# Optimization experiments

Measured on AMD Instinct MI355X. Metric: run time of the kernel, lower is better.

The kernel has to match this reference:

```python
import jax, jax.numpy as jnp
import numpy as np

IN_DIM = 5000
OUT_DIM = 30
K = 50
BATCH = 16384


def setup_inputs() -> dict:
    key = jax.random.key(0)
    ks = jax.random.split(key, 8)
    return {
        "x": jax.random.normal(ks[0], (BATCH, IN_DIM), dtype=jnp.float32),
        "logits": jax.random.normal(ks[1], (IN_DIM,), dtype=jnp.float32),
        "W1": jax.random.normal(ks[2], (IN_DIM, 32), dtype=jnp.float32) * (1.0 / np.sqrt(IN_DIM)),
        "b1": jax.random.normal(ks[3], (32,), dtype=jnp.float32) * 0.01,
        "W2": jax.random.normal(ks[4], (32, 16), dtype=jnp.float32) * (1.0 / np.sqrt(32)),
        "b2": jax.random.normal(ks[5], (16,), dtype=jnp.float32) * 0.01,
        "W3": jax.random.normal(ks[6], (16, OUT_DIM), dtype=jnp.float32) * (1.0 / np.sqrt(16)),
        "b3": jax.random.normal(ks[7], (OUT_DIM,), dtype=jnp.float32) * 0.01,
        "epoch": 10,
        "total_epochs": 100,
    }


def reference(x, logits, W1, b1, W2, b2, W3, b3, epoch, total_epochs):
    # Eval path (training=False): top-k one-hot mask over the learned logits.
    # indices of top-k logits -> k-hot mask of shape [in_dim]
    _, idx = jax.lax.top_k(logits, K)                 # [K]
    mask = jnp.zeros_like(logits).at[idx].set(1.0)    # [in_dim], k-hot
    xm = mask * x                                      # [B, in_dim] gated input
    h = jax.nn.relu(xm @ W1 + b1)                      # [B, 32]
    h = jax.nn.relu(h @ W2 + b2)                       # [B, 16]
    out = h @ W3 + b3                                  # [B, out_dim]
    return out, mask
```

## Files before the change

### kernel.cpp

```cpp
#include <hip/hip_runtime.h>
#include <hip/hip_bf16.h>

#define N_IN 5000
#define K_SEL 50
#define B_ROWS 16384
#define OUT_D 30

__global__ __launch_bounds__(256) void topk_mask_kernel(
    const float* __restrict__ logits,
    float* __restrict__ mask,
    int* __restrict__ idx_out)
{
    __shared__ unsigned int s_cnt[36];
    __shared__ int s_tick, s_sel;

    const int tid  = threadIdx.x;
    const int lane = tid & 63;

    if (tid < 36) s_cnt[tid] = 0u;
    if (tid == 40) s_tick = 0;
    if (tid == 41) s_sel = 0;

    unsigned int key[20];
#pragma unroll
    for (int j = 0; j < 20; j++) {
        int i = tid + j * 256;
        if (i < N_IN) {
            unsigned int b = __float_as_uint(logits[i]);
            key[j] = (b & 0x80000000u) ? ~b : (b | 0x80000000u);
            mask[i] = 0.0f;
        } else {
            key[j] = 0u;
        }
    }
    __syncthreads();

    unsigned int lo = 0u, hi = 0xFFFFFFFFu;
    bool exact = false;
    unsigned int T;
    for (int iter = 0; iter < 32; iter++) {
        if (lo >= hi) break;
        unsigned int mid = lo + ((hi - lo) >> 1) + 1u;
        unsigned int c = 0;
#pragma unroll
        for (int j = 0; j < 20; j++) c += (key[j] >= mid) ? 1u : 0u;
#pragma unroll
        for (int off = 32; off > 0; off >>= 1) c += __shfl_down(c, off, 64);
        if (lane == 0) atomicAdd(&s_cnt[iter], c);
        __syncthreads();
        unsigned int cnt = s_cnt[iter];
        if (cnt == (unsigned)K_SEL) { T = mid; exact = true; break; }
        if (cnt > (unsigned)K_SEL) lo = mid; else hi = mid - 1u;
    }

    if (exact) {
#pragma unroll
        for (int j = 0; j < 20; j++) {
            int i = tid + j * 256;
            if (i < N_IN && key[j] >= T) {
                int slot = atomicAdd(&s_sel, 1);
                idx_out[slot] = i;
                mask[i] = 1.0f;
            }
        }
        return;
    }

    const unsigned int KT = lo;
    {
        unsigned int c = 0;
#pragma unroll
        for (int j = 0; j < 20; j++) c += (key[j] > KT) ? 1u : 0u;
#pragma unroll
        for (int off = 32; off > 0; off >>= 1) c += __shfl_down(c, off, 64);
        if (lane == 0) atomicAdd(&s_cnt[35], c);
    }
    __syncthreads();
    const int rem = K_SEL - (int)s_cnt[35];

#pragma unroll
    for (int j = 0; j < 20; j++) {
        int i = tid + j * 256;
        if (i >= N_IN) continue;
        unsigned int k = key[j];
        bool sel = false;
        if (k > KT) sel = true;
        else if (k == KT) { int t = atomicAdd(&s_tick, 1); sel = (t < rem); }
        if (sel) {
            int slot = atomicAdd(&s_sel, 1);
            idx_out[slot] = i;
            mask[i] = 1.0f;
        }
    }
}

__global__ __launch_bounds__(256) void gated_mlp_kernel(
    const float* __restrict__ x,
    const float* __restrict__ W1,
    const float* __restrict__ b1,
    const float* __restrict__ W2,
    const float* __restrict__ b2,
    const float* __restrict__ W3,
    const float* __restrict__ b3,
    const int* __restrict__ idx,
    float* __restrict__ out)
{
    __shared__ float xs[64 * 51];
    __shared__ float h1s[64 * 33];
    __shared__ float h2s[64 * 17];
    __shared__ float sW1[K_SEL * 32];
    __shared__ float sW2[32 * 16];
    __shared__ float sW3[16 * OUT_D];
    __shared__ float sb1[32];
    __shared__ float sb2[16];
    __shared__ float sb3[OUT_D];
    __shared__ int   sidx[K_SEL];

    const int tid = threadIdx.x;

    if (tid < K_SEL) sidx[tid] = idx[tid];
    for (int e = tid; e < K_SEL * 32; e += 256) {
        int k = e >> 5, j = e & 31;
        sW1[e] = W1[(size_t)idx[k] * 32 + j];
    }
    for (int e = tid; e < 32 * 16; e += 256) sW2[e] = W2[e];
    for (int e = tid; e < 16 * OUT_D; e += 256) sW3[e] = W3[e];
    if (tid < 32) sb1[tid] = b1[tid];
    if (tid < 16) sb2[tid] = b2[tid];
    if (tid < OUT_D) sb3[tid] = b3[tid];
    __syncthreads();

    {
        const int r = tid >> 2;
        const int q = tid & 3;
        const int row = blockIdx.x * 64 + r;
        const float* __restrict__ xrow = x + (size_t)row * N_IN;
        float g[13];
#pragma unroll
        for (int u = 0; u < 13; u++) {
            int k = q * 13 + u;
            if (k < K_SEL) g[u] = xrow[sidx[k]];
        }
#pragma unroll
        for (int u = 0; u < 13; u++) {
            int k = q * 13 + u;
            if (k < K_SEL) xs[r * 51 + k] = g[u];
        }
    }
    __syncthreads();

    const int r = tid & 63;
    const int c = tid >> 6;

    {
        float acc[8];
#pragma unroll
        for (int jj = 0; jj < 8; jj++) acc[jj] = sb1[c * 8 + jj];
        const float* xr = &xs[r * 51];
        for (int k = 0; k < K_SEL; k++) {
            float xk = xr[k];
            const float* w = &sW1[k * 32 + c * 8];
#pragma unroll
            for (int jj = 0; jj < 8; jj++) acc[jj] = fmaf(xk, w[jj], acc[jj]);
        }
#pragma unroll
        for (int jj = 0; jj < 8; jj++) h1s[r * 33 + c * 8 + jj] = fmaxf(acc[jj], 0.0f);
    }
    __syncthreads();

    {
        float acc[4];
#pragma unroll
        for (int jj = 0; jj < 4; jj++) acc[jj] = sb2[c * 4 + jj];
        const float* hr = &h1s[r * 33];
#pragma unroll
        for (int i = 0; i < 32; i++) {
            float a = hr[i];
            const float* w = &sW2[i * 16 + c * 4];
#pragma unroll
            for (int jj = 0; jj < 4; jj++) acc[jj] = fmaf(a, w[jj], acc[jj]);
        }
#pragma unroll
        for (int jj = 0; jj < 4; jj++) h2s[r * 17 + c * 4 + jj] = fmaxf(acc[jj], 0.0f);
    }
    __syncthreads();

    {
        const int j0 = c * 8;
        const int nj = (c == 3) ? 6 : 8;
        float acc[8];
        for (int jj = 0; jj < nj; jj++) acc[jj] = sb3[j0 + jj];
        const float* hr = &h2s[r * 17];
#pragma unroll
        for (int i = 0; i < 16; i++) {
            float a = hr[i];
            const float* w = &sW3[i * OUT_D + j0];
            for (int jj = 0; jj < nj; jj++) acc[jj] = fmaf(a, w[jj], acc[jj]);
        }
        float* so = xs;
        for (int jj = 0; jj < nj; jj++) so[r * OUT_D + j0 + jj] = acc[jj];
    }
    __syncthreads();

    {
        float4* out4 = (float4*)(out + (size_t)blockIdx.x * 64 * OUT_D);
        const float4* so4 = (const float4*)xs;
        for (int e = tid; e < (64 * OUT_D) / 4; e += 256) out4[e] = so4[e];
    }
}

extern "C" void kernel_launch(void* const* d_in, const int* in_sizes, int n_in,
                              void* d_out, int out_size, void* d_ws, size_t ws_size,
                              hipStream_t stream) {
    const float* x      = (const float*)d_in[0];
    const float* logits = (const float*)d_in[1];
    const float* W1     = (const float*)d_in[2];
    const float* b1     = (const float*)d_in[3];
    const float* W2     = (const float*)d_in[4];
    const float* b2     = (const float*)d_in[5];
    const float* W3     = (const float*)d_in[6];
    const float* b3     = (const float*)d_in[7];

    float* out  = (float*)d_out;
    float* mask = out + (size_t)B_ROWS * OUT_D;
    int*   idx  = (int*)d_ws;

    topk_mask_kernel<<<1, 256, 0, stream>>>(logits, mask, idx);
    gated_mlp_kernel<<<256, 256, 0, stream>>>(x, W1, b1, W2, b2, W3, b3, idx, out);
}
```

Measured before the change: 424.1 us.

## Fuse top-k selection into the MLP kernel, recomputing it per block

Measured after the change: 421.3 us. No clear change (-0.7%).

```diff
diff --git a/kernel.cpp b/kernel.cpp
--- a/kernel.cpp
+++ b/kernel.cpp
@@ -6,104 +6,17 @@
 #define B_ROWS 16384
 #define OUT_D 30
 
-__global__ __launch_bounds__(256) void topk_mask_kernel(
+__global__ __launch_bounds__(256) void fused_gated_mlp_kernel(
+    const float* __restrict__ x,
     const float* __restrict__ logits,
-    float* __restrict__ mask,
-    int* __restrict__ idx_out)
-{
-    __shared__ unsigned int s_cnt[36];
-    __shared__ int s_tick, s_sel;
-
-    const int tid  = threadIdx.x;
-    const int lane = tid & 63;
-
-    if (tid < 36) s_cnt[tid] = 0u;
-    if (tid == 40) s_tick = 0;
-    if (tid == 41) s_sel = 0;
-
-    unsigned int key[20];
-#pragma unroll
-    for (int j = 0; j < 20; j++) {
-        int i = tid + j * 256;
-        if (i < N_IN) {
-            unsigned int b = __float_as_uint(logits[i]);
-            key[j] = (b & 0x80000000u) ? ~b : (b | 0x80000000u);
-            mask[i] = 0.0f;
-        } else {
-            key[j] = 0u;
-        }
-    }
-    __syncthreads();
-
-    unsigned int lo = 0u, hi = 0xFFFFFFFFu;
-    bool exact = false;
-    unsigned int T;
-    for (int iter = 0; iter < 32; iter++) {
-        if (lo >= hi) break;
-        unsigned int mid = lo + ((hi - lo) >> 1) + 1u;
-        unsigned int c = 0;
-#pragma unroll
-        for (int j = 0; j < 20; j++) c += (key[j] >= mid) ? 1u : 0u;
-#pragma unroll
-        for (int off = 32; off > 0; off >>= 1) c += __shfl_down(c, off, 64);
-        if (lane == 0) atomicAdd(&s_cnt[iter], c);
-        __syncthreads();
-        unsigned int cnt = s_cnt[iter];
-        if (cnt == (unsigned)K_SEL) { T = mid; exact = true; break; }
-        if (cnt > (unsigned)K_SEL) lo = mid; else hi = mid - 1u;
-    }
-
-    if (exact) {
-#pragma unroll
-        for (int j = 0; j < 20; j++) {
-            int i = tid + j * 256;
-            if (i < N_IN && key[j] >= T) {
-                int slot = atomicAdd(&s_sel, 1);
-                idx_out[slot] = i;
-                mask[i] = 1.0f;
-            }
-        }
-        return;
-    }
-
-    const unsigned int KT = lo;
-    {
-        unsigned int c = 0;
-#pragma unroll
-        for (int j = 0; j < 20; j++) c += (key[j] > KT) ? 1u : 0u;
-#pragma unroll
-        for (int off = 32; off > 0; off >>= 1) c += __shfl_down(c, off, 64);
-        if (lane == 0) atomicAdd(&s_cnt[35], c);
-    }
-    __syncthreads();
-    const int rem = K_SEL - (int)s_cnt[35];
-
-#pragma unroll
-    for (int j = 0; j < 20; j++) {
-        int i = tid + j * 256;
-        if (i >= N_IN) continue;
-        unsigned int k = key[j];
-        bool sel = false;
-        if (k > KT) sel = true;
-        else if (k == KT) { int t = atomicAdd(&s_tick, 1); sel = (t < rem); }
-        if (sel) {
-            int slot = atomicAdd(&s_sel, 1);
-            idx_out[slot] = i;
-            mask[i] = 1.0f;
-        }
-    }
-}
-
-__global__ __launch_bounds__(256) void gated_mlp_kernel(
-    const float* __restrict__ x,
     const float* __restrict__ W1,
     const float* __restrict__ b1,
     const float* __restrict__ W2,
     const float* __restrict__ b2,
     const float* __restrict__ W3,
     const float* __restrict__ b3,
-    const int* __restrict__ idx,
-    float* __restrict__ out)
+    float* __restrict__ out,
+    float* __restrict__ mask)
 {
     __shared__ float xs[64 * 51];
     __shared__ float h1s[64 * 33];
@@ -115,21 +28,91 @@
     __shared__ float sb2[16];
     __shared__ float sb3[OUT_D];
     __shared__ int   sidx[K_SEL];
-
-    const int tid = threadIdx.x;
-
-    if (tid < K_SEL) sidx[tid] = idx[tid];
-    for (int e = tid; e < K_SEL * 32; e += 256) {
-        int k = e >> 5, j = e & 31;
-        sW1[e] = W1[(size_t)idx[k] * 32 + j];
-    }
+    __shared__ unsigned int s_cnt[36];
+    __shared__ int s_tick, s_sel;
+
+    const int tid  = threadIdx.x;
+    const int lane = tid & 63;
+
+    if (tid < 36) s_cnt[tid] = 0u;
+    if (tid == 40) s_tick = 0;
+    if (tid == 41) s_sel = 0;
+
     for (int e = tid; e < 32 * 16; e += 256) sW2[e] = W2[e];
     for (int e = tid; e < 16 * OUT_D; e += 256) sW3[e] = W3[e];
     if (tid < 32) sb1[tid] = b1[tid];
     if (tid < 16) sb2[tid] = b2[tid];
     if (tid < OUT_D) sb3[tid] = b3[tid];
-    __syncthreads();
-
+
+    unsigned int key[20];
+#pragma unroll
+    for (int j = 0; j < 20; j++) {
+        int i = tid + j * 256;
+        if (i < N_IN) {
+            unsigned int b = __float_as_uint(logits[i]);
+            key[j] = (b & 0x80000000u) ? ~b : (b | 0x80000000u);
+        } else {
+            key[j] = 0u;
+        }
+    }
+    __syncthreads();
+
+    unsigned int lo = 0u, hi = 0xFFFFFFFFu;
+    bool exact = false;
+    unsigned int T = 0;
+    for (int iter = 0; iter < 32; iter++) {
+        if (lo >= hi) break;
+        unsigned int mid = lo + ((hi - lo) >> 1) + 1u;
+        unsigned int c = 0;
+#pragma unroll
+        for (int j = 0; j < 20; j++) c += (key[j] >= mid) ? 1u : 0u;
+#pragma unroll
+        for (int off = 32; off > 0; off >>= 1) c += __shfl_down(c, off, 64);
+        if (lane == 0) atomicAdd(&s_cnt[iter], c);
+        __syncthreads();
+        unsigned int cnt = s_cnt[iter];
+        if (cnt == (unsigned)K_SEL) { T = mid; exact = true; break; }
+        if (cnt > (unsigned)K_SEL) lo = mid; else hi = mid - 1u;
+    }
+
+    const bool write_mask = (blockIdx.x == 0);
+    if (exact) {
+#pragma unroll
+        for (int j = 0; j < 20; j++) {
+            int i = tid + j * 256;
+            if (i >= N_IN) continue;
+            bool sel = (key[j] >= T);
+            if (sel) { int s = atomicAdd(&s_sel, 1); sidx[s] = i; }
+            if (write_mask) mask[i] = sel ? 1.0f : 0.0f;
+        }
+    } else {
+        const unsigned int KT = lo;
+        unsigned int c = 0;
+#pragma unroll
+        for (int j = 0; j < 20; j++) c += (key[j] > KT) ? 1u : 0u;
+#pragma unroll
+        for (int off = 32; off > 0; off >>= 1) c += __shfl_down(c, off, 64);
+        if (lane == 0) atomicAdd(&s_cnt[35], c);
+        __syncthreads();
+        const int rem = K_SEL - (int)s_cnt[35];
+#pragma unroll
+        for (int j = 0; j < 20; j++) {
+            int i = tid + j * 256;
+            if (i >= N_IN) continue;
+            unsigned int k = key[j];
+            bool sel = false;
+            if (k > KT) sel = true;
+            else if (k == KT) { int t = atomicAdd(&s_tick, 1); sel = (t < rem); }
+            if (sel) { int s = atomicAdd(&s_sel, 1); sidx[s] = i; }
+            if (write_mask) mask[i] = sel ? 1.0f : 0.0f;
+        }
+    }
+    __syncthreads();
+
+    for (int e = tid; e < K_SEL * 32; e += 256) {
+        int k = e >> 5, j = e & 31;
+        sW1[e] = W1[(size_t)sidx[k] * 32 + j];
+    }
     {
         const int r = tid >> 2;
         const int q = tid & 3;
@@ -223,8 +206,7 @@
 
     float* out  = (float*)d_out;
     float* mask = out + (size_t)B_ROWS * OUT_D;
-    int*   idx  = (int*)d_ws;
-
-    topk_mask_kernel<<<1, 256, 0, stream>>>(logits, mask, idx);
-    gated_mlp_kernel<<<256, 256, 0, stream>>>(x, W1, b1, W2, b2, W3, b3, idx, out);
+
+    fused_gated_mlp_kernel<<<256, 256, 0, stream>>>(
+        x, logits, W1, b1, W2, b2, W3, b3, out, mask);
 }
```
